# Performance work log

Measured on AMD Instinct MI355X. Metric: run time of the kernel, lower is better.

## Reference

```python
import jax, jax.numpy as jnp
import numpy as np

N = 100000      # nodes
E = 1600000     # edges (before self-loops)
IN = 128        # in_dim
HID = 128       # hidden_dim
H = 4           # heads
D = HID // H    # head_dim = 32
L = 3           # n_layers
G = 128         # graphs in batch
NEG_SLOPE = 0.2 # PyG GATConv default leaky_relu slope
BN_EPS = 1e-5


def setup_inputs() -> dict:
    key = jax.random.key(0)
    ks = jax.random.split(key, 16)
    x = jax.random.normal(ks[0], (N, IN), dtype=jnp.float32)
    edge_index = jax.random.randint(ks[1], (2, E), 0, N, dtype=jnp.int64)
    batch = jnp.sort(jax.random.randint(ks[2], (N,), 0, G, dtype=jnp.int64))
    # stacked per-layer GATConv params (in_dim == hidden_dim so all layers stack)
    W = jax.random.normal(ks[3], (L, HID, HID), dtype=jnp.float32) * (1.0 / np.sqrt(HID))
    att_src = jax.random.normal(ks[4], (L, H, D), dtype=jnp.float32) * 0.1
    att_dst = jax.random.normal(ks[5], (L, H, D), dtype=jnp.float32) * 0.1
    bias = jax.random.normal(ks[6], (L, HID), dtype=jnp.float32) * 0.01
    # BatchNorm1d (eval mode: running stats)
    gamma = 1.0 + 0.1 * jax.random.normal(ks[7], (L, HID), dtype=jnp.float32)
    beta = 0.01 * jax.random.normal(ks[8], (L, HID), dtype=jnp.float32)
    bn_mean = jnp.zeros((L, HID), dtype=jnp.float32)
    bn_var = jnp.ones((L, HID), dtype=jnp.float32)
    # MLP head: Linear(HID, HID//2) -> ReLU -> Linear(HID//2, 1)
    Wh1 = jax.random.normal(ks[9], (HID, HID // 2), dtype=jnp.float32) * (1.0 / np.sqrt(HID))
    bh1 = jnp.zeros((HID // 2,), dtype=jnp.float32)
    Wh2 = jax.random.normal(ks[10], (HID // 2, 1), dtype=jnp.float32) * (1.0 / np.sqrt(HID // 2))
    bh2 = jnp.zeros((1,), dtype=jnp.float32)
    return {"x": x, "edge_index": edge_index, "batch": batch, "W": W,
            "att_src": att_src, "att_dst": att_dst, "bias": bias,
            "gamma": gamma, "beta": beta, "bn_mean": bn_mean, "bn_var": bn_var,
            "Wh1": Wh1, "bh1": bh1, "Wh2": Wh2, "bh2": bh2}


def _gat_conv(x, src, dst, W_l, asrc, adst, b):
    # x: [N, F_in]; src/dst: [E+N] (self-loops included); returns [N, H*D]
    h = (x @ W_l).reshape(N, H, D)                      # [N,H,D]
    a_s = jnp.einsum('nhd,hd->nh', h, asrc)             # [N,H]
    a_d = jnp.einsum('nhd,hd->nh', h, adst)
    e = jax.nn.leaky_relu(a_s[src] + a_d[dst], NEG_SLOPE)  # [Etot,H]
    # segment softmax over incoming edges per destination node
    e_max = jax.ops.segment_max(e, dst, num_segments=N)    # [N,H]
    p = jnp.exp(e - e_max[dst])
    denom = jax.ops.segment_sum(p, dst, num_segments=N)    # [N,H]
    alpha = p / (denom[dst] + 1e-16)                        # [Etot,H]
    msg = h[src] * alpha[:, :, None]                        # [Etot,H,D]
    out = jax.ops.segment_sum(msg, dst, num_segments=N)     # [N,H,D]
    return out.reshape(N, H * D) + b


def reference(x, edge_index, batch, W, att_src, att_dst, bias,
              gamma, beta, bn_mean, bn_var, Wh1, bh1, Wh2, bh2):
    # add self-loops once (PyG GATConv default add_self_loops=True)
    loop = jnp.arange(N, dtype=edge_index.dtype)
    src = jnp.concatenate([edge_index[0], loop])
    dst = jnp.concatenate([edge_index[1], loop])
    for l in range(L):
        x = _gat_conv(x, src, dst, W[l], att_src[l], att_dst[l], bias[l])
        x = jnp.maximum(x, 0.0)
        # BatchNorm1d, eval mode (dropout is identity in eval)
        x = (x - bn_mean[l]) * (gamma[l] / jnp.sqrt(bn_var[l] + BN_EPS)) + beta[l]
    # global mean pool over graphs
    sums = jax.ops.segment_sum(x, batch, num_segments=G)            # [G,HID]
    cnts = jax.ops.segment_sum(jnp.ones((N,), x.dtype), batch, num_segments=G)
    pooled = sums / jnp.maximum(cnts, 1.0)[:, None]
    hdn = jnp.maximum(pooled @ Wh1 + bh1, 0.0)
    return (hdn @ Wh2 + bh2).squeeze(-1)                            # [G]
```

## Files before the change

### kernel.cpp

```cpp
#include <hip/hip_runtime.h>
#include <hip/hip_fp16.h>


typedef __bf16 bf16x8 __attribute__((ext_vector_type(8)));
typedef float  f32x4  __attribute__((ext_vector_type(4)));
typedef unsigned int u32x4 __attribute__((ext_vector_type(4)));

#define WLSZ 36864
#define MAXBKT 800
#define BCAP   4096

__global__ __launch_bounds__(256)
void k_bucket(const int* __restrict__ ei, unsigned int* __restrict__ bkt,
              int* __restrict__ bcnt, float* __restrict__ gsum,
              int* __restrict__ gcnt, int Ne, int Nn, int nbkt, int Gg) {
    __shared__ int lcnt[MAXBKT];
    __shared__ int lbase[MAXBKT];
    int tid = threadIdx.x;
    int gid = blockIdx.x * 256 + tid;
    if (gid < Gg * 128) gsum[gid] = 0.f;
    if (gid < Gg) gcnt[gid] = 0;
    for (int i = tid; i < nbkt; i += 256) lcnt[i] = 0;
    __syncthreads();
    int chunk0 = blockIdx.x * 2048;
    int nnz = Ne + Nn;
    for (int i = 0; i < 8; ++i) {
        int e = chunk0 + i * 256 + tid;
        if (e < nnz) {
            int d = (e < Ne) ? ei[Ne + e] : (e - Ne);
            atomicAdd(&lcnt[d >> 7], 1);
        }
    }
    __syncthreads();
    for (int b = tid; b < nbkt; b += 256) {
        int c = lcnt[b];
        lbase[b] = (c > 0) ? atomicAdd(&bcnt[b], c) : 0;
        lcnt[b] = 0;
    }
    __syncthreads();
    for (int i = 0; i < 8; ++i) {
        int e = chunk0 + i * 256 + tid;
        if (e < nnz) {
            int s, d;
            if (e < Ne) { s = ei[e]; d = ei[Ne + e]; }
            else        { s = e - Ne; d = e - Ne; }
            int b = d >> 7;
            int r = atomicAdd(&lcnt[b], 1);
            bkt[(long)b * BCAP + lbase[b] + r] = ((unsigned)s << 7) | (unsigned)(d & 127);
        }
    }
}

__global__ __launch_bounds__(1024)
void k_bktscan(const int* __restrict__ bcnt, int* __restrict__ bktbase, int nbkt) {
    __shared__ int s0[1024], s1[1024];
    int t = threadIdx.x;
    int v = (t < nbkt) ? bcnt[t] : 0;
    s0[t] = v;
    __syncthreads();
    int* src = s0; int* dst = s1;
    for (int off = 1; off < 1024; off <<= 1) {
        int x = src[t];
        if (t >= off) x += src[t - off];
        dst[t] = x;
        __syncthreads();
        int* tw = src; src = dst; dst = tw;
    }
    if (t < nbkt) bktbase[t] = src[t] - v;
}

__global__ __launch_bounds__(256)
void k_bscatter2(const unsigned int* __restrict__ bkt, const int* __restrict__ bcnt,
                 const int* __restrict__ bktbase, int* __restrict__ rowptr,
                 int* __restrict__ colv, int Nn, int nnz) {
    __shared__ int h[128], sc0[128], sc1[128];
    int b = blockIdx.x;
    int tid = threadIdx.x;
    if (tid < 128) h[tid] = 0;
    __syncthreads();
    int cnt = bcnt[b];
    int base = bktbase[b];
    const unsigned int* bp = bkt + (long)b * BCAP;
    for (int i = tid; i < cnt; i += 256) atomicAdd(&h[bp[i] & 127], 1);
    __syncthreads();
    if (tid < 128) sc0[tid] = h[tid];
    __syncthreads();
    int* src = sc0; int* dst = sc1;
    for (int off = 1; off < 128; off <<= 1) {
        if (tid < 128) {
            int x = src[tid];
            if (tid >= off) x += src[tid - off];
            dst[tid] = x;
        }
        __syncthreads();
        int* tw = src; src = dst; dst = tw;
    }
    int node = b * 128 + tid;
    if (tid < 128) {
        int excl = src[tid] - h[tid];
        int st = base + excl;
        h[tid] = st;
        if (node < Nn) rowptr[node] = st;
    }
    if (b == 0 && tid == 0) rowptr[Nn] = nnz;
    __syncthreads();
    for (int i = tid; i < cnt; i += 256) {
        unsigned int e = bp[i];
        int pos = atomicAdd(&h[e & 127], 1);
        colv[pos] = (int)(e >> 7);
    }
}

__global__ __launch_bounds__(128)
void k_gcnt(const int* __restrict__ batch, int* __restrict__ gcnt, int Nn, int Gg) {
    int g = threadIdx.x;
    if (g >= Gg) return;
    int lo = 0, hi = Nn;
    while (lo < hi) { int mid = (lo + hi) >> 1; if (batch[mid] < g) lo = mid + 1; else hi = mid; }
    int lo2 = lo, hi2 = Nn;
    while (lo2 < hi2) { int mid = (lo2 + hi2) >> 1; if (batch[mid] < g + 1) lo2 = mid + 1; else hi2 = mid; }
    gcnt[g] = lo2 - lo;
}

__device__ __forceinline__ int foff(int l, int d, int n, int k) {
    int ct = n >> 4, li = n & 15;
    int ks = k >> 5, bq = (k >> 3) & 3, j = k & 7;
    return l * WLSZ + (((ks * 18) + d * 9 + ct) * 64 + (bq << 4) + li) * 8 + j;
}

__global__ void k_prep(const float* __restrict__ gamma, const float* __restrict__ beta,
                       const float* __restrict__ mean, const float* __restrict__ var,
                       float* __restrict__ bn_mul, float* __restrict__ bn_add,
                       const float* __restrict__ W, const float* __restrict__ asrc,
                       const float* __restrict__ adst, __bf16* __restrict__ WF) {
    int gid = blockIdx.x * 256 + threadIdx.x;
    if (gid < 384) {
        float sc = gamma[gid] / sqrtf(var[gid] + 1e-5f);
        bn_mul[gid] = sc;
        bn_add[gid] = beta[gid] - mean[gid] * sc;
    }
    if (gid < 3 * 128 * 128) {
        int l = gid >> 14;
        int k = (gid >> 7) & 127;
        int n = gid & 127;
        float f = W[gid];
        __bf16 h = (__bf16)f;
        WF[foff(l, 0, n, k)] = h;
        WF[foff(l, 1, n, k)] = (__bf16)(f - (float)h);
    }
    if (gid < 3 * 128 * 8) {
        int l = gid >> 10;
        int r = gid & 1023;
        int k = r >> 3;
        int j = r & 7;
        int hh = j & 3;
        const float* av = (j < 4 ? asrc : adst) + l * 128 + hh * 32;
        const float* wp = W + l * 16384 + k * 128 + hh * 32;
        float sum = 0.f;
#pragma unroll
        for (int d = 0; d < 32; ++d) sum = fmaf(wp[d], av[d], sum);
        __bf16 h = (__bf16)sum;
        WF[foff(l, 0, 128 + j, k)] = h;
        WF[foff(l, 1, 128 + j, k)] = (__bf16)(sum - (float)h);
    }
    if (gid < 3 * 128 * 8) {
        int l = gid >> 10;
        int r = gid & 1023;
        int k = r >> 3;
        int j = r & 7;
        WF[foff(l, 0, 136 + j, k)] = (__bf16)0.f;
        WF[foff(l, 1, 136 + j, k)] = (__bf16)0.f;
    }
}

__global__ __launch_bounds__(256, 4)
void k_gemm_mfma(const float* __restrict__ X, const __bf16* __restrict__ WF,
                 __half* __restrict__ Hout,
                 float* __restrict__ as_, float* __restrict__ ad_, int Nn) {
    int t = threadIdx.x;
    int w = t >> 6;
    int lane = t & 63;
    int li = lane & 15;
    int b  = lane >> 4;
    long row = (long)blockIdx.x * 64 + w * 16 + li;
    long rA = (row > Nn - 1) ? (Nn - 1) : row;

    f32x4 acc[9];
#pragma unroll
    for (int ct = 0; ct < 9; ++ct) acc[ct] = (f32x4){0.f, 0.f, 0.f, 0.f};

#pragma unroll
    for (int ks = 0; ks < 4; ++ks) {
        int k0 = ks * 32 + 8 * b;
        const float* xp = X + rA * 128 + k0;
        float4 f0 = *(const float4*)xp;
        float4 f1 = *(const float4*)(xp + 4);
        float af[8] = {f0.x, f0.y, f0.z, f0.w, f1.x, f1.y, f1.z, f1.w};
        bf16x8 ahi, alo;
#pragma unroll
        for (int j = 0; j < 8; ++j) {
            __bf16 h = (__bf16)af[j];
            ahi[j] = h;
            alo[j] = (__bf16)(af[j] - (float)h);
        }
        const __bf16* wk = WF + (ks * 18) * 512 + lane * 8;
#pragma unroll
        for (int ct = 0; ct < 9; ++ct) {
            bf16x8 bhi = *(const bf16x8*)(wk + ct * 512);
            bf16x8 blo = *(const bf16x8*)(wk + (9 + ct) * 512);
            acc[ct] = __builtin_amdgcn_mfma_f32_16x16x32_bf16(bhi, ahi, acc[ct], 0, 0, 0);
            acc[ct] = __builtin_amdgcn_mfma_f32_16x16x32_bf16(bhi, alo, acc[ct], 0, 0, 0);
            acc[ct] = __builtin_amdgcn_mfma_f32_16x16x32_bf16(blo, ahi, acc[ct], 0, 0, 0);
        }
    }

    if (row < Nn) {
        __half* op = Hout + row * 128 + 4 * b;
#pragma unroll
        for (int ct = 0; ct < 8; ++ct) {
            union { __half2 h2[2]; uint2 u; } pk;
            pk.h2[0] = __floats2half2_rn(acc[ct][0], acc[ct][1]);
            pk.h2[1] = __floats2half2_rn(acc[ct][2], acc[ct][3]);
            *(uint2*)(op + ct * 16) = pk.u;
        }
        if (b == 0)
            *(float4*)(as_ + 4 * row) = make_float4(acc[8][0], acc[8][1],
                                                    acc[8][2], acc[8][3]);
        else if (b == 1)
            *(float4*)(ad_ + 4 * row) = make_float4(acc[8][0], acc[8][1],
                                                    acc[8][2], acc[8][3]);
    }
}

#define LEAKY(x) ((x) > 0.f ? (x) : 0.2f * (x))

template <bool POOL>
__global__ __launch_bounds__(256)
void k_aggregate(const __half* __restrict__ Hb, const float* __restrict__ as_,
                 const float* __restrict__ ad_, const int* __restrict__ rowptr,
                 const int* __restrict__ col, const float* __restrict__ bias,
                 const float* __restrict__ bn_mul, const float* __restrict__ bn_add,
                 float* __restrict__ Xout, const int* __restrict__ batch,
                 float* __restrict__ gsum, int Nn) {
    __shared__ int2 s_pk[4][64][4];
    __shared__ float s_out[POOL ? 4 : 1][POOL ? 128 : 1];
    __shared__ int s_g[POOL ? 4 : 1];
    int w = threadIdx.x >> 6;
    int n = (blockIdx.x << 2) + w;
    int lane = threadIdx.x & 63;
    bool active = (n < Nn);
    if (!POOL && !active) return;
    if (POOL && lane == 0) s_g[w] = active ? batch[n] : -1;

    if (active) {
        int start = rowptr[n], end = rowptr[n + 1];
        int deg = end - start;

        if (deg <= 64) {
            int hh = lane & 3;
            int slot = lane >> 2;
            float adn = ad_[4 * n + hh];
            float esc[4]; int scl[4];
#pragma unroll
            for (int c = 0; c < 4; ++c) {
                int eidx = (c << 4) + slot;
                float e = -1e30f; int s = 0;
                if (eidx < deg) {
                    s = col[start + eidx];
                    e = LEAKY(as_[4 * s + hh] + adn);
                }
                esc[c] = e; scl[c] = s;
            }
            float m = fmaxf(fmaxf(esc[0], esc[1]), fmaxf(esc[2], esc[3]));
#pragma unroll
            for (int msk = 4; msk < 64; msk <<= 1) m = fmaxf(m, __shfl_xor(m, msk, 64));
            float p[4];
            float den = 0.f;
#pragma unroll
            for (int c = 0; c < 4; ++c) { p[c] = __expf(esc[c] - m); den += p[c]; }
#pragma unroll
            for (int msk = 4; msk < 64; msk <<= 1) den += __shfl_xor(den, msk, 64);
            float inv = 1.f / (den + 1e-16f);
#pragma unroll
            for (int c = 0; c < 4; ++c) {
                int2 pk;
                pk.x = scl[c] << 8;
                pk.y = __float_as_int(p[c] * inv);
                s_pk[w][(c << 4) + slot][hh] = pk;
            }

            int quarter = lane >> 4;
            int li = lane & 15;
            int hB = li >> 2;
            int cByte = li << 4;
            const char* hb8 = (const char*)Hb;
            float acc[8];
#pragma unroll
            for (int i = 0; i < 8; ++i) acc[i] = 0.f;

            int nit = (deg + 7) >> 3;
            int2 pk0 = s_pk[w][quarter][hB];
            int2 pk1 = s_pk[w][quarter + 4][hB];
            float a0 = __int_as_float(pk0.y);
            float a1 = __int_as_float(pk1.y);
            u32x4 r0 = *(const u32x4*)(hb8 + pk0.x + cByte);
            u32x4 r1 = *(const u32x4*)(hb8 + pk1.x + cByte);
            for (int it = 1; it < nit; ++it) {
                int e0 = (it << 3) + quarter;
                int2 q0 = s_pk[w][e0][hB];
                int2 q1 = s_pk[w][e0 + 4][hB];
                u32x4 t0 = *(const u32x4*)(hb8 + q0.x + cByte);
                u32x4 t1 = *(const u32x4*)(hb8 + q1.x + cByte);
                const __half* h0 = (const __half*)&r0;
                const __half* h1 = (const __half*)&r1;
#pragma unroll
                for (int q = 0; q < 8; ++q) {
                    acc[q] = fmaf(__half2float(h0[q]), a0, acc[q]);
                    acc[q] = fmaf(__half2float(h1[q]), a1, acc[q]);
                }
                r0 = t0; r1 = t1;
                a0 = __int_as_float(q0.y);
                a1 = __int_as_float(q1.y);
            }
            {
                const __half* h0 = (const __half*)&r0;
                const __half* h1 = (const __half*)&r1;
#pragma unroll
                for (int q = 0; q < 8; ++q) {
                    acc[q] = fmaf(__half2float(h0[q]), a0, acc[q]);
                    acc[q] = fmaf(__half2float(h1[q]), a1, acc[q]);
                }
            }
#pragma unroll
            for (int i = 0; i < 8; ++i) {
                float v = acc[i];
                v += __shfl_xor(v, 16, 64);
                v += __shfl_xor(v, 32, 64);
                acc[i] = v;
            }
            if (lane < 16) {
                int c0 = li << 3;
                float4 bz0 = *(const float4*)(bias + c0);
                float4 bz1 = *(const float4*)(bias + c0 + 4);
                float4 m0 = *(const float4*)(bn_mul + c0);
                float4 m1 = *(const float4*)(bn_mul + c0 + 4);
                float4 a0v = *(const float4*)(bn_add + c0);
                float4 a1v = *(const float4*)(bn_add + c0 + 4);
                float4 o0, o1;
                o0.x = fmaf(fmaxf(acc[0] + bz0.x, 0.f), m0.x, a0v.x);
                o0.y = fmaf(fmaxf(acc[1] + bz0.y, 0.f), m0.y, a0v.y);
                o0.z = fmaf(fmaxf(acc[2] + bz0.z, 0.f), m0.z, a0v.z);
                o0.w = fmaf(fmaxf(acc[3] + bz0.w, 0.f), m0.w, a0v.w);
                o1.x = fmaf(fmaxf(acc[4] + bz1.x, 0.f), m1.x, a1v.x);
                o1.y = fmaf(fmaxf(acc[5] + bz1.y, 0.f), m1.y, a1v.y);
                o1.z = fmaf(fmaxf(acc[6] + bz1.z, 0.f), m1.z, a1v.z);
                o1.w = fmaf(fmaxf(acc[7] + bz1.w, 0.f), m1.w, a1v.w);
                if (!POOL) {
                    *(float4*)(Xout + (long)n * 128 + c0)     = o0;
                    *(float4*)(Xout + (long)n * 128 + c0 + 4) = o1;
                } else {
                    *(float4*)(&s_out[w][c0])     = o0;
                    *(float4*)(&s_out[w][c0 + 4]) = o1;
                }
            }
        } else {
            int hh = lane & 3;
            float adn = ad_[n * 4 + hh];
            float m = -1e30f;
            for (int base = start; base < end; base += 16) {
                int idx = base + (lane >> 2);
                float sc = -1e30f;
                if (idx < end) {
                    int s = col[idx];
                    float e = as_[s * 4 + hh] + adn;
                    sc = LEAKY(e);
                }
                m = fmaxf(m, sc);
            }
            for (int msk = 4; msk < 64; msk <<= 1) m = fmaxf(m, __shfl_xor(m, msk, 64));
            float den = 0.f;
            for (int base = start; base < end; base += 16) {
                int idx = base + (lane >> 2);
                if (idx < end) {
                    int s = col[idx];
                    float e = as_[s * 4 + hh] + adn;
                    e = LEAKY(e);
                    den += __expf(e - m);
                }
            }
            for (int msk = 4; msk < 64; msk <<= 1) den += __shfl_xor(den, msk, 64);
            int hB = lane >> 4;
            float mB   = __shfl(m, hB, 64);
            float invB = 1.f / (__shfl(den, hB, 64) + 1e-16f);
            float adB  = ad_[n * 4 + hB];
            int c0 = lane << 1;
            float acc0 = 0.f, acc1 = 0.f;
            for (int i = start; i < end; ++i) {
                int s = col[i];
                float e = as_[s * 4 + hB] + adB;
                e = LEAKY(e);
                float alpha = __expf(e - mB) * invB;
                float2 hv = __half22float2(*(const __half2*)(Hb + (long)s * 128 + c0));
                acc0 = fmaf(hv.x, alpha, acc0);
                acc1 = fmaf(hv.y, alpha, acc1);
            }
            float v0 = acc0 + bias[c0], v1 = acc1 + bias[c0 + 1];
            v0 = fmaxf(v0, 0.f); v1 = fmaxf(v1, 0.f);
            v0 = fmaf(v0, bn_mul[c0], bn_add[c0]);
            v1 = fmaf(v1, bn_mul[c0 + 1], bn_add[c0 + 1]);
            if (!POOL) {
                *(float2*)(Xout + (long)n * 128 + c0) = make_float2(v0, v1);
            } else {
                s_out[w][c0]     = v0;
                s_out[w][c0 + 1] = v1;
            }
        }
    } else if (POOL) {
        if (lane < 16) {
            int c0 = (lane & 15) << 3;
#pragma unroll
            for (int i = 0; i < 8; ++i) s_out[w][c0 + i] = 0.f;
        }
    }

    if (POOL) {
        __syncthreads();
        int tid = threadIdx.x;
        if (tid < 128) {
            int g0 = s_g[0], g1 = s_g[1], g2 = s_g[2], g3 = s_g[3];
            float v0 = s_out[0][tid], v1 = s_out[1][tid];
            float v2 = s_out[2][tid], v3 = s_out[3][tid];
            if (g0 == g1 && g1 == g2 && g2 == g3) {
                if (g0 >= 0) atomicAdd(&gsum[g0 * 128 + tid], v0 + v1 + v2 + v3);
            } else {
                if (g0 >= 0) atomicAdd(&gsum[g0 * 128 + tid], v0);
                if (g1 >= 0) atomicAdd(&gsum[g1 * 128 + tid], v1);
                if (g2 >= 0) atomicAdd(&gsum[g2 * 128 + tid], v2);
                if (g3 >= 0) atomicAdd(&gsum[g3 * 128 + tid], v3);
            }
        }
    }
}

__global__ __launch_bounds__(64)
void k_head(const float* __restrict__ gsum, const int* __restrict__ gcnt,
            const float* __restrict__ Wh1, const float* __restrict__ bh1,
            const float* __restrict__ Wh2, const float* __restrict__ bh2,
            float* __restrict__ outp) {
    __shared__ float pooled[128];
    int g = blockIdx.x;
    int j = threadIdx.x;
    int cnt = gcnt[g];
    float inv = 1.f / (float)(cnt > 1 ? cnt : 1);
    pooled[j]      = gsum[g * 128 + j] * inv;
    pooled[j + 64] = gsum[g * 128 + 64 + j] * inv;
    __syncthreads();
    float acc = bh1[j];
    for (int k = 0; k < 128; ++k) acc = fmaf(pooled[k], Wh1[k * 64 + j], acc);
    acc = fmaxf(acc, 0.f);
    float prod = acc * Wh2[j];
    for (int msk = 1; msk < 64; msk <<= 1) prod += __shfl_xor(prod, msk, 64);
    if (j == 0) outp[g] = prod + bh2[0];
}

extern "C" void kernel_launch(void* const* d_in, const int* in_sizes, int n_in,
                              void* d_out, int out_size, void* d_ws, size_t ws_size,
                              hipStream_t stream) {
    const float* x       = (const float*)d_in[0];
    const int*   ei      = (const int*)d_in[1];
    const int*   batch   = (const int*)d_in[2];
    const float* W       = (const float*)d_in[3];
    const float* att_src = (const float*)d_in[4];
    const float* att_dst = (const float*)d_in[5];
    const float* bias    = (const float*)d_in[6];
    const float* gamma   = (const float*)d_in[7];
    const float* beta    = (const float*)d_in[8];
    const float* bn_mean = (const float*)d_in[9];
    const float* bn_var  = (const float*)d_in[10];
    const float* Wh1     = (const float*)d_in[11];
    const float* bh1     = (const float*)d_in[12];
    const float* Wh2     = (const float*)d_in[13];
    const float* bh2     = (const float*)d_in[14];
    float* out = (float*)d_out;

    const int Nn = in_sizes[0] / 128;
    const int Ne = in_sizes[1] / 2;
    const int Gg = out_size;
    const int nnz = Ne + Nn;
    const int nbkt = (Nn + 127) / 128;

    char* ws = (char*)d_ws;
    size_t off = 0;
    auto alloc = [&](size_t bytes) -> char* {
        char* p = ws + off;
        off = (off + bytes + 255) & ~(size_t)255;
        return p;
    };
    float*        bufA    = (float*)alloc((size_t)Nn * 128 * 4);
    __half*       bufH    = (__half*)alloc((size_t)Nn * 128 * 2);
    float*        as_     = (float*)alloc((size_t)Nn * 4 * 4);
    float*        ad_     = (float*)alloc((size_t)Nn * 4 * 4);
    int*          rowptr  = (int*)alloc((size_t)(Nn + 1) * 4);
    int*          col     = (int*)alloc((size_t)nnz * 4);
    float*        bn_mul  = (float*)alloc(384 * 4);
    float*        bn_add  = (float*)alloc(384 * 4);
    float*        gsum    = (float*)alloc((size_t)Gg * 128 * 4);
    int*          gcnt    = (int*)alloc((size_t)Gg * 4);
    __bf16*       WtF     = (__bf16*)alloc((size_t)3 * WLSZ * 2);
    unsigned int* bkt     = (unsigned int*)alloc((size_t)nbkt * BCAP * 4);
    int*          bcnt    = (int*)alloc((size_t)nbkt * 4);
    int*          bktbase = (int*)alloc((size_t)nbkt * 4);

    hipMemsetAsync(bcnt, 0, (size_t)nbkt * 4, stream);
    k_prep<<<192, 256, 0, stream>>>(gamma, beta, bn_mean, bn_var, bn_mul, bn_add,
                                    W, att_src, att_dst, WtF);
    k_bucket<<<(nnz + 2047) / 2048, 256, 0, stream>>>(ei, bkt, bcnt, gsum, gcnt,
                                                      Ne, Nn, nbkt, Gg);
    k_gcnt<<<1, 128, 0, stream>>>(batch, gcnt, Nn, Gg);
    k_bktscan<<<1, 1024, 0, stream>>>(bcnt, bktbase, nbkt);
    k_bscatter2<<<nbkt, 256, 0, stream>>>(bkt, bcnt, bktbase, rowptr, col, Nn, nnz);

    const float* cur = x;
    for (int l = 0; l < 3; ++l) {
        k_gemm_mfma<<<(Nn + 63) / 64, 256, 0, stream>>>(cur, WtF + l * WLSZ,
                                                        bufH, as_, ad_, Nn);
        if (l < 2)
            k_aggregate<false><<<(Nn + 3) / 4, 256, 0, stream>>>(
                bufH, as_, ad_, rowptr, col, bias + l * 128, bn_mul + l * 128,
                bn_add + l * 128, bufA, batch, gsum, Nn);
        else
            k_aggregate<true><<<(Nn + 3) / 4, 256, 0, stream>>>(
                bufH, as_, ad_, rowptr, col, bias + l * 128, bn_mul + l * 128,
                bn_add + l * 128, bufA, batch, gsum, Nn);
        cur = bufA;
    }

    k_head<<<Gg, 64, 0, stream>>>(gsum, gcnt, Wh1, bh1, Wh2, bh2, out);
}
```

Measured before the change: 525.3 us.

## Merge front-end prep kernels and drop bucket scan via padded CSR

Fuses the weight/BN prep, edge bucketing and per-graph count kernels into one launch, with disjoint block ranges doing each job. Removes the single-block bucket prefix scan by laying the CSR column array out in fixed per-bucket slots (BCAP stride). Rows are then described by a start offset and a degree instead of rowptr. This cuts the number of serialized launches and one tiny serial kernel, at the cost of a larger, padded col array and less contiguous neighbor lists across buckets.

Result: faster. 504.2 us (-4.0%).

```diff
diff --git a/kernel.cpp b/kernel.cpp
--- a/kernel.cpp
+++ b/kernel.cpp
@@ -10,80 +10,125 @@
 #define MAXBKT 800
 #define BCAP   4096
 
+__device__ __forceinline__ int foff(int l, int d, int n, int k) {
+    int ct = n >> 4, li = n & 15;
+    int ks = k >> 5, bq = (k >> 3) & 3, j = k & 7;
+    return l * WLSZ + (((ks * 18) + d * 9 + ct) * 64 + (bq << 4) + li) * 8 + j;
+}
+
 __global__ __launch_bounds__(256)
-void k_bucket(const int* __restrict__ ei, unsigned int* __restrict__ bkt,
-              int* __restrict__ bcnt, float* __restrict__ gsum,
-              int* __restrict__ gcnt, int Ne, int Nn, int nbkt, int Gg) {
+void k_front(const int* __restrict__ ei, unsigned int* __restrict__ bkt,
+             int* __restrict__ bcnt, float* __restrict__ gsum,
+             int* __restrict__ gcnt, const int* __restrict__ batch,
+             const float* __restrict__ gamma, const float* __restrict__ beta,
+             const float* __restrict__ mean, const float* __restrict__ var,
+             float* __restrict__ bn_mul, float* __restrict__ bn_add,
+             const float* __restrict__ W, const float* __restrict__ asrc,
+             const float* __restrict__ adst, __bf16* __restrict__ WF,
+             int Ne, int Nn, int nbkt, int Gg, int nBB) {
     __shared__ int lcnt[MAXBKT];
     __shared__ int lbase[MAXBKT];
+    int bb = blockIdx.x;
     int tid = threadIdx.x;
-    int gid = blockIdx.x * 256 + tid;
-    if (gid < Gg * 128) gsum[gid] = 0.f;
-    if (gid < Gg) gcnt[gid] = 0;
-    for (int i = tid; i < nbkt; i += 256) lcnt[i] = 0;
-    __syncthreads();
-    int chunk0 = blockIdx.x * 2048;
-    int nnz = Ne + Nn;
-    for (int i = 0; i < 8; ++i) {
-        int e = chunk0 + i * 256 + tid;
-        if (e < nnz) {
-            int d = (e < Ne) ? ei[Ne + e] : (e - Ne);
-            atomicAdd(&lcnt[d >> 7], 1);
-        }
-    }
-    __syncthreads();
-    for (int b = tid; b < nbkt; b += 256) {
-        int c = lcnt[b];
-        lbase[b] = (c > 0) ? atomicAdd(&bcnt[b], c) : 0;
-        lcnt[b] = 0;
-    }
-    __syncthreads();
-    for (int i = 0; i < 8; ++i) {
-        int e = chunk0 + i * 256 + tid;
-        if (e < nnz) {
-            int s, d;
-            if (e < Ne) { s = ei[e]; d = ei[Ne + e]; }
-            else        { s = e - Ne; d = e - Ne; }
-            int b = d >> 7;
-            int r = atomicAdd(&lcnt[b], 1);
-            bkt[(long)b * BCAP + lbase[b] + r] = ((unsigned)s << 7) | (unsigned)(d & 127);
-        }
-    }
-}
-
-__global__ __launch_bounds__(1024)
-void k_bktscan(const int* __restrict__ bcnt, int* __restrict__ bktbase, int nbkt) {
-    __shared__ int s0[1024], s1[1024];
-    int t = threadIdx.x;
-    int v = (t < nbkt) ? bcnt[t] : 0;
-    s0[t] = v;
-    __syncthreads();
-    int* src = s0; int* dst = s1;
-    for (int off = 1; off < 1024; off <<= 1) {
-        int x = src[t];
-        if (t >= off) x += src[t - off];
-        dst[t] = x;
+
+    if (bb < nBB) {
+        int gid = bb * 256 + tid;
+        if (gid < Gg * 128) gsum[gid] = 0.f;
+        for (int i = tid; i < nbkt; i += 256) lcnt[i] = 0;
         __syncthreads();
-        int* tw = src; src = dst; dst = tw;
-    }
-    if (t < nbkt) bktbase[t] = src[t] - v;
+        int chunk0 = bb * 2048;
+        int nnz = Ne + Nn;
+        for (int i = 0; i < 8; ++i) {
+            int e = chunk0 + i * 256 + tid;
+            if (e < nnz) {
+                int d = (e < Ne) ? ei[Ne + e] : (e - Ne);
+                atomicAdd(&lcnt[d >> 7], 1);
+            }
+        }
+        __syncthreads();
+        for (int b = tid; b < nbkt; b += 256) {
+            int c = lcnt[b];
+            lbase[b] = (c > 0) ? atomicAdd(&bcnt[b], c) : 0;
+            lcnt[b] = 0;
+        }
+        __syncthreads();
+        for (int i = 0; i < 8; ++i) {
+            int e = chunk0 + i * 256 + tid;
+            if (e < nnz) {
+                int s, d;
+                if (e < Ne) { s = ei[e]; d = ei[Ne + e]; }
+                else        { s = e - Ne; d = e - Ne; }
+                int b = d >> 7;
+                int r = atomicAdd(&lcnt[b], 1);
+                bkt[(long)b * BCAP + lbase[b] + r] = ((unsigned)s << 7) | (unsigned)(d & 127);
+            }
+        }
+    } else if (bb < nBB + 192) {
+        int gid = (bb - nBB) * 256 + tid;
+        if (gid < 384) {
+            float sc = gamma[gid] / sqrtf(var[gid] + 1e-5f);
+            bn_mul[gid] = sc;
+            bn_add[gid] = beta[gid] - mean[gid] * sc;
+        }
+        if (gid < 3 * 128 * 128) {
+            int l = gid >> 14;
+            int k = (gid >> 7) & 127;
+            int n = gid & 127;
+            float f = W[gid];
+            __bf16 h = (__bf16)f;
+            WF[foff(l, 0, n, k)] = h;
+            WF[foff(l, 1, n, k)] = (__bf16)(f - (float)h);
+        }
+        if (gid < 3 * 128 * 8) {
+            int l = gid >> 10;
+            int r = gid & 1023;
+            int k = r >> 3;
+            int j = r & 7;
+            int hh = j & 3;
+            const float* av = (j < 4 ? asrc : adst) + l * 128 + hh * 32;
+            const float* wp = W + l * 16384 + k * 128 + hh * 32;
+            float sum = 0.f;
+#pragma unroll
+            for (int d = 0; d < 32; ++d) sum = fmaf(wp[d], av[d], sum);
+            __bf16 h = (__bf16)sum;
+            WF[foff(l, 0, 128 + j, k)] = h;
+            WF[foff(l, 1, 128 + j, k)] = (__bf16)(sum - (float)h);
+        }
+        if (gid < 3 * 128 * 8) {
+            int l = gid >> 10;
+            int r = gid & 1023;
+            int k = r >> 3;
+            int j = r & 7;
+            WF[foff(l, 0, 136 + j, k)] = (__bf16)0.f;
+            WF[foff(l, 1, 136 + j, k)] = (__bf16)0.f;
+        }
+    } else {
+        int g = tid;
+        if (g < Gg) {
+            int lo = 0, hi = Nn;
+            while (lo < hi) { int mid = (lo + hi) >> 1; if (batch[mid] < g) lo = mid + 1; else hi = mid; }
+            int lo2 = lo, hi2 = Nn;
+            while (lo2 < hi2) { int mid = (lo2 + hi2) >> 1; if (batch[mid] < g + 1) lo2 = mid + 1; else hi2 = mid; }
+            gcnt[g] = lo2 - lo;
+        }
+    }
 }
 
 __global__ __launch_bounds__(256)
 void k_bscatter2(const unsigned int* __restrict__ bkt, const int* __restrict__ bcnt,
-                 const int* __restrict__ bktbase, int* __restrict__ rowptr,
-                 int* __restrict__ colv, int Nn, int nnz) {
+                 int* __restrict__ rowstart, int* __restrict__ rowdeg,
+                 int* __restrict__ colv, int Nn) {
     __shared__ int h[128], sc0[128], sc1[128];
     int b = blockIdx.x;
     int tid = threadIdx.x;
     if (tid < 128) h[tid] = 0;
     __syncthreads();
     int cnt = bcnt[b];
-    int base = bktbase[b];
     const unsigned int* bp = bkt + (long)b * BCAP;
     for (int i = tid; i < cnt; i += 256) atomicAdd(&h[bp[i] & 127], 1);
     __syncthreads();
-    if (tid < 128) sc0[tid] = h[tid];
+    int cntN = (tid < 128) ? h[tid] : 0;
+    if (tid < 128) sc0[tid] = cntN;
     __syncthreads();
     int* src = sc0; int* dst = sc1;
     for (int off = 1; off < 128; off <<= 1) {
@@ -97,79 +142,15 @@
     }
     int node = b * 128 + tid;
     if (tid < 128) {
-        int excl = src[tid] - h[tid];
-        int st = base + excl;
+        int st = b * BCAP + (src[tid] - cntN);
         h[tid] = st;
-        if (node < Nn) rowptr[node] = st;
-    }
-    if (b == 0 && tid == 0) rowptr[Nn] = nnz;
+        if (node < Nn) { rowstart[node] = st; rowdeg[node] = cntN; }
+    }
     __syncthreads();
     for (int i = tid; i < cnt; i += 256) {
         unsigned int e = bp[i];
         int pos = atomicAdd(&h[e & 127], 1);
         colv[pos] = (int)(e >> 7);
-    }
-}
-
-__global__ __launch_bounds__(128)
-void k_gcnt(const int* __restrict__ batch, int* __restrict__ gcnt, int Nn, int Gg) {
-    int g = threadIdx.x;
-    if (g >= Gg) return;
-    int lo = 0, hi = Nn;
-    while (lo < hi) { int mid = (lo + hi) >> 1; if (batch[mid] < g) lo = mid + 1; else hi = mid; }
-    int lo2 = lo, hi2 = Nn;
-    while (lo2 < hi2) { int mid = (lo2 + hi2) >> 1; if (batch[mid] < g + 1) lo2 = mid + 1; else hi2 = mid; }
-    gcnt[g] = lo2 - lo;
-}
-
-__device__ __forceinline__ int foff(int l, int d, int n, int k) {
-    int ct = n >> 4, li = n & 15;
-    int ks = k >> 5, bq = (k >> 3) & 3, j = k & 7;
-    return l * WLSZ + (((ks * 18) + d * 9 + ct) * 64 + (bq << 4) + li) * 8 + j;
-}
-
-__global__ void k_prep(const float* __restrict__ gamma, const float* __restrict__ beta,
-                       const float* __restrict__ mean, const float* __restrict__ var,
-                       float* __restrict__ bn_mul, float* __restrict__ bn_add,
-                       const float* __restrict__ W, const float* __restrict__ asrc,
-                       const float* __restrict__ adst, __bf16* __restrict__ WF) {
-    int gid = blockIdx.x * 256 + threadIdx.x;
-    if (gid < 384) {
-        float sc = gamma[gid] / sqrtf(var[gid] + 1e-5f);
-        bn_mul[gid] = sc;
-        bn_add[gid] = beta[gid] - mean[gid] * sc;
-    }
-    if (gid < 3 * 128 * 128) {
-        int l = gid >> 14;
-        int k = (gid >> 7) & 127;
-        int n = gid & 127;
-        float f = W[gid];
-        __bf16 h = (__bf16)f;
-        WF[foff(l, 0, n, k)] = h;
-        WF[foff(l, 1, n, k)] = (__bf16)(f - (float)h);
-    }
-    if (gid < 3 * 128 * 8) {
-        int l = gid >> 10;
-        int r = gid & 1023;
-        int k = r >> 3;
-        int j = r & 7;
-        int hh = j & 3;
-        const float* av = (j < 4 ? asrc : adst) + l * 128 + hh * 32;
-        const float* wp = W + l * 16384 + k * 128 + hh * 32;
-        float sum = 0.f;
-#pragma unroll
-        for (int d = 0; d < 32; ++d) sum = fmaf(wp[d], av[d], sum);
-        __bf16 h = (__bf16)sum;
-        WF[foff(l, 0, 128 + j, k)] = h;
-        WF[foff(l, 1, 128 + j, k)] = (__bf16)(sum - (float)h);
-    }
-    if (gid < 3 * 128 * 8) {
-        int l = gid >> 10;
-        int r = gid & 1023;
-        int k = r >> 3;
-        int j = r & 7;
-        WF[foff(l, 0, 136 + j, k)] = (__bf16)0.f;
-        WF[foff(l, 1, 136 + j, k)] = (__bf16)0.f;
     }
 }
 
@@ -237,7 +218,8 @@
 template <bool POOL>
 __global__ __launch_bounds__(256)
 void k_aggregate(const __half* __restrict__ Hb, const float* __restrict__ as_,
-                 const float* __restrict__ ad_, const int* __restrict__ rowptr,
+                 const float* __restrict__ ad_, const int* __restrict__ rowstart,
+                 const int* __restrict__ rowdeg,
                  const int* __restrict__ col, const float* __restrict__ bias,
                  const float* __restrict__ bn_mul, const float* __restrict__ bn_add,
                  float* __restrict__ Xout, const int* __restrict__ batch,
@@ -253,8 +235,8 @@
     if (POOL && lane == 0) s_g[w] = active ? batch[n] : -1;
 
     if (active) {
-        int start = rowptr[n], end = rowptr[n + 1];
-        int deg = end - start;
+        int start = rowstart[n];
+        int deg = rowdeg[n];
 
         if (deg <= 64) {
             int hh = lane & 3;
@@ -364,6 +346,7 @@
                 }
             }
         } else {
+            int end = start + deg;
             int hh = lane & 3;
             float adn = ad_[n * 4 + hh];
             float m = -1e30f;
@@ -488,6 +471,7 @@
     const int Gg = out_size;
     const int nnz = Ne + Nn;
     const int nbkt = (Nn + 127) / 128;
+    const int nBB = (nnz + 2047) / 2048;
 
     char* ws = (char*)d_ws;
     size_t off = 0;
@@ -496,29 +480,27 @@
         off = (off + bytes + 255) & ~(size_t)255;
         return p;
     };
-    float*        bufA    = (float*)alloc((size_t)Nn * 128 * 4);
-    __half*       bufH    = (__half*)alloc((size_t)Nn * 128 * 2);
-    float*        as_     = (float*)alloc((size_t)Nn * 4 * 4);
-    float*        ad_     = (float*)alloc((size_t)Nn * 4 * 4);
-    int*          rowptr  = (int*)alloc((size_t)(Nn + 1) * 4);
-    int*          col     = (int*)alloc((size_t)nnz * 4);
-    float*        bn_mul  = (float*)alloc(384 * 4);
-    float*        bn_add  = (float*)alloc(384 * 4);
-    float*        gsum    = (float*)alloc((size_t)Gg * 128 * 4);
-    int*          gcnt    = (int*)alloc((size_t)Gg * 4);
-    __bf16*       WtF     = (__bf16*)alloc((size_t)3 * WLSZ * 2);
-    unsigned int* bkt     = (unsigned int*)alloc((size_t)nbkt * BCAP * 4);
-    int*          bcnt    = (int*)alloc((size_t)nbkt * 4);
-    int*          bktbase = (int*)alloc((size_t)nbkt * 4);
+    float*        bufA     = (float*)alloc((size_t)Nn * 128 * 4);
+    __half*       bufH     = (__half*)alloc((size_t)Nn * 128 * 2);
+    float*        as_      = (float*)alloc((size_t)Nn * 4 * 4);
+    float*        ad_      = (float*)alloc((size_t)Nn * 4 * 4);
+    int*          rowstart = (int*)alloc((size_t)Nn * 4);
+    int*          rowdeg   = (int*)alloc((size_t)Nn * 4);
+    int*          col      = (int*)alloc((size_t)nbkt * BCAP * 4);
+    float*        bn_mul   = (float*)alloc(384 * 4);
+    float*        bn_add   = (float*)alloc(384 * 4);
+    float*        gsum     = (float*)alloc((size_t)Gg * 128 * 4);
+    int*          gcnt     = (int*)alloc((size_t)Gg * 4);
+    __bf16*       WtF      = (__bf16*)alloc((size_t)3 * WLSZ * 2);
+    unsigned int* bkt      = (unsigned int*)alloc((size_t)nbkt * BCAP * 4);
+    int*          bcnt     = (int*)alloc((size_t)nbkt * 4);
 
     hipMemsetAsync(bcnt, 0, (size_t)nbkt * 4, stream);
-    k_prep<<<192, 256, 0, stream>>>(gamma, beta, bn_mean, bn_var, bn_mul, bn_add,
-                                    W, att_src, att_dst, WtF);
-    k_bucket<<<(nnz + 2047) / 2048, 256, 0, stream>>>(ei, bkt, bcnt, gsum, gcnt,
-                                                      Ne, Nn, nbkt, Gg);
-    k_gcnt<<<1, 128, 0, stream>>>(batch, gcnt, Nn, Gg);
-    k_bktscan<<<1, 1024, 0, stream>>>(bcnt, bktbase, nbkt);
-    k_bscatter2<<<nbkt, 256, 0, stream>>>(bkt, bcnt, bktbase, rowptr, col, Nn, nnz);
+    k_front<<<nBB + 193, 256, 0, stream>>>(ei, bkt, bcnt, gsum, gcnt, batch,
+                                           gamma, beta, bn_mean, bn_var,
+                                           bn_mul, bn_add, W, att_src, att_dst,
+                                           WtF, Ne, Nn, nbkt, Gg, nBB);
+    k_bscatter2<<<nbkt, 256, 0, stream>>>(bkt, bcnt, rowstart, rowdeg, col, Nn);
 
     const float* cur = x;
     for (int l = 0; l < 3; ++l) {
@@ -526,12 +508,12 @@
                                                         bufH, as_, ad_, Nn);
         if (l < 2)
             k_aggregate<false><<<(Nn + 3) / 4, 256, 0, stream>>>(
-                bufH, as_, ad_, rowptr, col, bias + l * 128, bn_mul + l * 128,
-                bn_add + l * 128, bufA, batch, gsum, Nn);
+                bufH, as_, ad_, rowstart, rowdeg, col, bias + l * 128,
+                bn_mul + l * 128, bn_add + l * 128, bufA, batch, gsum, Nn);
         else
             k_aggregate<true><<<(Nn + 3) / 4, 256, 0, stream>>>(
-                bufH, as_, ad_, rowptr, col, bias + l * 128, bn_mul + l * 128,
-                bn_add + l * 128, bufA, batch, gsum, Nn);
+                bufH, as_, ad_, rowstart, rowdeg, col, bias + l * 128,
+                bn_mul + l * 128, bn_add + l * 128, bufA, batch, gsum, Nn);
         cur = bufA;
     }
 
```
